# Performance work log

Measured on AMD Instinct MI355X. Metric: run time of the kernel, lower is better.

Reference implementation:

```python
import jax, jax.numpy as jnp
import numpy as np

B, L, C, H, W = 2, 16, 16, 64, 64


def setup_inputs() -> dict:
    key = jax.random.key(0)
    k1, k2 = jax.random.split(key)
    # flows scaled so cumulative normalized-coordinate flows mostly stay in [-1, 1]
    flows = jax.random.normal(k1, (B, L, 2, H, W), dtype=jnp.float32) * 0.05
    images = jax.random.normal(k2, (B, L, C, H, W), dtype=jnp.float32)
    return {"flows": flows, "images": images}


def _bilinear_sample(images, gx, gy):
    # images: [B, Lj, C, H, W]; gx, gy: [B, Li, Lj, H, W] normalized coords in [-1, 1]
    # Replicates torch.nn.functional.grid_sample(mode='bilinear',
    # padding_mode='zeros', align_corners=False).
    Bs, Lj, Cs, Hs, Ws = images.shape
    ix = ((gx + 1.0) * Ws - 1.0) * 0.5  # pixel x coord
    iy = ((gy + 1.0) * Hs - 1.0) * 0.5  # pixel y coord
    x0f = jnp.floor(ix)
    y0f = jnp.floor(iy)
    wx = ix - x0f  # weight toward x0+1 (differentiable w.r.t. flow)
    wy = iy - y0f
    x0 = x0f.astype(jnp.int32)
    y0 = y0f.astype(jnp.int32)
    img_flat = images.reshape(Bs, Lj, Cs, Hs * Ws)

    def gather(xi, yi):
        valid = (xi >= 0) & (xi < Ws) & (yi >= 0) & (yi < Hs)  # [B,Li,Lj,H,W]
        lin = jnp.clip(yi, 0, Hs - 1) * Ws + jnp.clip(xi, 0, Ws - 1)
        lin_t = jnp.transpose(lin, (0, 2, 1, 3, 4))  # [B,Lj,Li,H,W]
        # per (b, j): gather [C, HW] at indices [Li, H, W] -> [C, Li, H, W]
        v = jax.vmap(jax.vmap(lambda im, l: im[:, l]))(img_flat, lin_t)
        v = jnp.transpose(v, (0, 3, 1, 2, 4, 5))  # [B,Li,Lj,C,H,W]
        return v * valid[:, :, :, None, :, :].astype(v.dtype)

    v00 = gather(x0, y0)
    v01 = gather(x0 + 1, y0)
    v10 = gather(x0, y0 + 1)
    v11 = gather(x0 + 1, y0 + 1)
    wX = wx[:, :, :, None, :, :]
    wY = wy[:, :, :, None, :, :]
    return (v00 * (1.0 - wX) * (1.0 - wY) + v01 * wX * (1.0 - wY)
            + v10 * (1.0 - wX) * wY + v11 * wX * wY)


def reference(flows, images):
    Bs, Ls, _, Hs, Ws = flows.shape
    dt = flows.dtype
    cum = jnp.cumsum(flows, axis=1)  # [B,L,2,H,W]
    # rel[b, i, j] = cum[b, i] - cum[b, j]  -> [B,Li,Lj,2,H,W]
    rel = cum[:, :, None] - cum[:, None, :]
    # base sampling grid (pixel centers in normalized coords)
    gx_base = (jnp.arange(Ws, dtype=dt) + 0.5) * (2.0 / Ws) - 1.0  # [W]
    gy_base = (jnp.arange(Hs, dtype=dt) + 0.5) * (2.0 / Hs) - 1.0  # [H]
    gx = gx_base + rel[:, :, :, 0]              # [B,Li,Lj,H,W]
    gy = gy_base[:, None] + rel[:, :, :, 1]     # [B,Li,Lj,H,W]
    gx = jnp.remainder(gx + 1.0, 2.0) - 1.0     # wrap x into [-1, 1)
    warped = _bilinear_sample(images, gx, gy)   # [B,Li,Lj,C,H,W]
    mask = jnp.tril(jnp.ones((Ls, Ls), dtype=dt))
    # causal accumulate over source index j
    return jnp.einsum('bijchw,ij->bichw', warped, mask)
```

## Files before the change

### kernel.cpp

```cpp
#include <hip/hip_runtime.h>

#define BB 2
#define LL 16
#define CC 16
#define HH 64
#define WW 64
#define HWSZ (HH * WW)
#define NSEG 36

__device__ __constant__ int SEG_I[NSEG] = {
    1, 2, 3, 4,
    5, 5, 6, 6, 7, 7, 8, 8,
    9, 9, 9, 10, 10, 10, 11, 11, 11, 12, 12, 12,
    13, 13, 13, 13, 14, 14, 14, 14, 15, 15, 15, 15};
__device__ __constant__ int SEG_J0[NSEG] = {
    0, 0, 0, 0,
    0, 4, 0, 4, 0, 4, 0, 4,
    0, 4, 8, 0, 4, 8, 0, 4, 8, 0, 4, 8,
    0, 4, 8, 12, 0, 4, 8, 12, 0, 4, 8, 12};

#define CUM2_FLOATS (BB * LL * HWSZ * 2)

__global__ __launch_bounds__(256) void gsp_prep(
    const float* __restrict__ flows,
    const float* __restrict__ images,
    float2* __restrict__ cum2,
    float4* __restrict__ nhwc,
    float* __restrict__ out)
{
    if (blockIdx.x < 32) {
        const int gid = blockIdx.x * 256 + threadIdx.x;
        const int b   = gid >> 12;
        const int pix = gid & (HWSZ - 1);
        const float* fb = flows + (size_t)b * LL * 2 * HWSZ + pix;
        float vx[LL], vy[LL];
        #pragma unroll
        for (int l = 0; l < LL; ++l) {
            vx[l] = fb[(size_t)l * 2 * HWSZ];
            vy[l] = fb[(size_t)l * 2 * HWSZ + HWSZ];
        }
        #pragma unroll
        for (int l = 1; l < LL; ++l) { vx[l] += vx[l - 1]; vy[l] += vy[l - 1]; }
        float2* cb = cum2 + (size_t)b * LL * HWSZ + pix;
        #pragma unroll
        for (int l = 0; l < LL; ++l) {
            float2 v; v.x = vx[l]; v.y = vy[l];
            cb[(size_t)l * HWSZ] = v;
        }
    } else {
        const int gid  = (blockIdx.x - 32) * 256 + threadIdx.x;
        const int quad = gid & 3;
        const int pix  = (gid >> 2) & (HWSZ - 1);
        const int bl   = gid >> 14;

        const float* src = images + (size_t)(bl * CC + quad * 4) * HWSZ + pix;
        float4 v;
        v.x = src[0 * HWSZ];
        v.y = src[1 * HWSZ];
        v.z = src[2 * HWSZ];
        v.w = src[3 * HWSZ];
        nhwc[(size_t)(bl * HWSZ + pix) * 4 + quad] = v;

        float* op = out + (size_t)(bl * CC + quad * 4) * HWSZ + pix;
        op[0 * HWSZ] = v.x;
        op[1 * HWSZ] = v.y;
        op[2 * HWSZ] = v.z;
        op[3 * HWSZ] = v.w;
    }
}

__global__ __launch_bounds__(256) void gsp_pairs(
    const float2* __restrict__ cum2,
    const float* __restrict__ nhwc,
    float* __restrict__ out)
{
    const int tile = blockIdx.x & 63;
    const int seg  = (blockIdx.x >> 6) % NSEG;
    const int b    = blockIdx.x / (64 * NSEG);

    const int i    = SEG_I[seg];
    const int j0   = SEG_J0[seg];
    const int jmax = i - 1;

    const int psub = threadIdx.x >> 2;
    const int quad = threadIdx.x & 3;
    const int pix  = tile * 64 + psub;
    const int h = pix >> 6;
    const int w = pix & (WW - 1);

    const float2* cum_b = cum2 + (size_t)b * LL * HWSZ + pix;
    const float* nhwc_b = nhwc + (size_t)b * LL * HWSZ * CC;

    const float gxb = (w + 0.5f) * (2.0f / WW) - 1.0f;
    const float gyb = (h + 0.5f) * (2.0f / HH) - 1.0f;

    const float2 ci = cum_b[(size_t)i * HWSZ];

    float ax = 0.0f, ay = 0.0f, az = 0.0f, aw = 0.0f;

    #pragma unroll
    for (int k = 0; k < 4; ++k) {
        const int jraw = j0 + k;
        const int j = min(jraw, jmax);
        const float wpad = (jraw <= jmax) ? 1.0f : 0.0f;

        const float2 cj = cum_b[(size_t)j * HWSZ];

        float gx = gxb + (ci.x - cj.x);
        float gy = gyb + (ci.y - cj.y);

        float tt = gx + 1.0f;
        tt = tt - floorf(tt * 0.5f) * 2.0f;
        gx = tt - 1.0f;

        const float ix = ((gx + 1.0f) * WW - 1.0f) * 0.5f;
        const float iy = ((gy + 1.0f) * HH - 1.0f) * 0.5f;
        const float x0f = floorf(ix);
        const float y0f = floorf(iy);
        const float fx = ix - x0f;
        const float fy = iy - y0f;
        const int x0 = (int)x0f;
        const int y0 = (int)y0f;
        const int x1 = x0 + 1;
        const int y1 = y0 + 1;

        const bool vx0 = (x0 >= 0) && (x0 < WW);
        const bool vx1 = (x1 >= 0) && (x1 < WW);
        const bool vy0 = (y0 >= 0) && (y0 < HH);
        const bool vy1 = (y1 >= 0) && (y1 < HH);

        const int cx0 = min(max(x0, 0), WW - 1);
        const int cx1 = min(max(x1, 0), WW - 1);
        const int cy0 = min(max(y0, 0), HH - 1);
        const int cy1 = min(max(y1, 0), HH - 1);

        const float w00 = wpad * (1.0f - fx) * (1.0f - fy) * ((vx0 && vy0) ? 1.0f : 0.0f);
        const float w01 = wpad * fx * (1.0f - fy)          * ((vx1 && vy0) ? 1.0f : 0.0f);
        const float w10 = wpad * (1.0f - fx) * fy          * ((vx0 && vy1) ? 1.0f : 0.0f);
        const float w11 = wpad * fx * fy                   * ((vx1 && vy1) ? 1.0f : 0.0f);

        const int o00 = cy0 * WW + cx0;
        const int o01 = cy0 * WW + cx1;
        const int o10 = cy1 * WW + cx0;
        const int o11 = cy1 * WW + cx1;

        const float4* jb = (const float4*)(nhwc_b + (size_t)j * HWSZ * CC);
        const float4 v00 = jb[o00 * 4 + quad];
        const float4 v01 = jb[o01 * 4 + quad];
        const float4 v10 = jb[o10 * 4 + quad];
        const float4 v11 = jb[o11 * 4 + quad];

        ax += w00 * v00.x + w01 * v01.x + w10 * v10.x + w11 * v11.x;
        ay += w00 * v00.y + w01 * v01.y + w10 * v10.y + w11 * v11.y;
        az += w00 * v00.z + w01 * v01.z + w10 * v10.z + w11 * v11.z;
        aw += w00 * v00.w + w01 * v01.w + w10 * v10.w + w11 * v11.w;
    }

    float* op = out + ((size_t)(b * LL + i) * CC + quad * 4) * HWSZ + pix;
    atomicAdd(op + 0 * HWSZ, ax);
    atomicAdd(op + 1 * HWSZ, ay);
    atomicAdd(op + 2 * HWSZ, az);
    atomicAdd(op + 3 * HWSZ, aw);
}

extern "C" void kernel_launch(void* const* d_in, const int* in_sizes, int n_in,
                              void* d_out, int out_size, void* d_ws, size_t ws_size,
                              hipStream_t stream) {
    const float* flows  = (const float*)d_in[0];
    const float* images = (const float*)d_in[1];
    float* out = (float*)d_out;
    float2* cum2 = (float2*)d_ws;
    float*  nhwc = (float*)d_ws + CUM2_FLOATS;

    gsp_prep<<<32 + 2048, 256, 0, stream>>>(flows, images, cum2, (float4*)nhwc, out);

    const int grid = BB * NSEG * 64;
    gsp_pairs<<<grid, 256, 0, stream>>>(cum2, nhwc, out);
}
```

Measured before the change: 91.84 us.

## Stage each source image quarter-plane in LDS and bilinear-gather from shared memory

The pair kernel is replaced by a segment kernel in which each 1024-thread block owns one (batch, target frame, 4-frame source segment, channel quad). For each source frame it copies a 64KB quarter-plane into LDS and does the four bilinear taps from shared memory instead of global/L2. The prep kernel now writes a plane-major quad layout so the block copy is a contiguous stream. In exchange the grid shrinks to 288 large blocks with heavy LDS use and a barrier per source frame. That gives low occupancy, no overlap between the copy and the compute, and a possible tail imbalance across CUs.

```diff
diff --git a/kernel.cpp b/kernel.cpp
--- a/kernel.cpp
+++ b/kernel.cpp
@@ -25,7 +25,7 @@
     const float* __restrict__ flows,
     const float* __restrict__ images,
     float2* __restrict__ cum2,
-    float4* __restrict__ nhwc,
+    float4* __restrict__ qp,
     float* __restrict__ out)
 {
     if (blockIdx.x < 32) {
@@ -59,7 +59,7 @@
         v.y = src[1 * HWSZ];
         v.z = src[2 * HWSZ];
         v.w = src[3 * HWSZ];
-        nhwc[(size_t)(bl * HWSZ + pix) * 4 + quad] = v;
+        qp[((size_t)bl * 4 + quad) * HWSZ + pix] = v;
 
         float* op = out + (size_t)(bl * CC + quad * 4) * HWSZ + pix;
         op[0 * HWSZ] = v.x;
@@ -69,98 +69,102 @@
     }
 }
 
-__global__ __launch_bounds__(256) void gsp_pairs(
+__global__ __launch_bounds__(1024, 8) void gsp_seg(
     const float2* __restrict__ cum2,
-    const float* __restrict__ nhwc,
+    const float4* __restrict__ qp,
     float* __restrict__ out)
 {
-    const int tile = blockIdx.x & 63;
-    const int seg  = (blockIdx.x >> 6) % NSEG;
-    const int b    = blockIdx.x / (64 * NSEG);
+    __shared__ float4 tile[HWSZ];
 
-    const int i    = SEG_I[seg];
-    const int j0   = SEG_J0[seg];
-    const int jmax = i - 1;
+    const int qs  = blockIdx.x & 3;
+    const int seg = (blockIdx.x >> 2) % NSEG;
+    const int b   = blockIdx.x / (4 * NSEG);
 
-    const int psub = threadIdx.x >> 2;
-    const int quad = threadIdx.x & 3;
-    const int pix  = tile * 64 + psub;
-    const int h = pix >> 6;
-    const int w = pix & (WW - 1);
+    const int i  = SEG_I[seg];
+    const int j0 = SEG_J0[seg];
+    const int j1 = min(j0 + 3, i - 1);
 
-    const float2* cum_b = cum2 + (size_t)b * LL * HWSZ + pix;
-    const float* nhwc_b = nhwc + (size_t)b * LL * HWSZ * CC;
+    const float2* cum_b = cum2 + (size_t)b * LL * HWSZ;
 
-    const float gxb = (w + 0.5f) * (2.0f / WW) - 1.0f;
-    const float gyb = (h + 0.5f) * (2.0f / HH) - 1.0f;
-
-    const float2 ci = cum_b[(size_t)i * HWSZ];
-
-    float ax = 0.0f, ay = 0.0f, az = 0.0f, aw = 0.0f;
-
+    float2 ci[4];
+    float4 acc[4];
     #pragma unroll
-    for (int k = 0; k < 4; ++k) {
-        const int jraw = j0 + k;
-        const int j = min(jraw, jmax);
-        const float wpad = (jraw <= jmax) ? 1.0f : 0.0f;
-
-        const float2 cj = cum_b[(size_t)j * HWSZ];
-
-        float gx = gxb + (ci.x - cj.x);
-        float gy = gyb + (ci.y - cj.y);
-
-        float tt = gx + 1.0f;
-        tt = tt - floorf(tt * 0.5f) * 2.0f;
-        gx = tt - 1.0f;
-
-        const float ix = ((gx + 1.0f) * WW - 1.0f) * 0.5f;
-        const float iy = ((gy + 1.0f) * HH - 1.0f) * 0.5f;
-        const float x0f = floorf(ix);
-        const float y0f = floorf(iy);
-        const float fx = ix - x0f;
-        const float fy = iy - y0f;
-        const int x0 = (int)x0f;
-        const int y0 = (int)y0f;
-        const int x1 = x0 + 1;
-        const int y1 = y0 + 1;
-
-        const bool vx0 = (x0 >= 0) && (x0 < WW);
-        const bool vx1 = (x1 >= 0) && (x1 < WW);
-        const bool vy0 = (y0 >= 0) && (y0 < HH);
-        const bool vy1 = (y1 >= 0) && (y1 < HH);
-
-        const int cx0 = min(max(x0, 0), WW - 1);
-        const int cx1 = min(max(x1, 0), WW - 1);
-        const int cy0 = min(max(y0, 0), HH - 1);
-        const int cy1 = min(max(y1, 0), HH - 1);
-
-        const float w00 = wpad * (1.0f - fx) * (1.0f - fy) * ((vx0 && vy0) ? 1.0f : 0.0f);
-        const float w01 = wpad * fx * (1.0f - fy)          * ((vx1 && vy0) ? 1.0f : 0.0f);
-        const float w10 = wpad * (1.0f - fx) * fy          * ((vx0 && vy1) ? 1.0f : 0.0f);
-        const float w11 = wpad * fx * fy                   * ((vx1 && vy1) ? 1.0f : 0.0f);
-
-        const int o00 = cy0 * WW + cx0;
-        const int o01 = cy0 * WW + cx1;
-        const int o10 = cy1 * WW + cx0;
-        const int o11 = cy1 * WW + cx1;
-
-        const float4* jb = (const float4*)(nhwc_b + (size_t)j * HWSZ * CC);
-        const float4 v00 = jb[o00 * 4 + quad];
-        const float4 v01 = jb[o01 * 4 + quad];
-        const float4 v10 = jb[o10 * 4 + quad];
-        const float4 v11 = jb[o11 * 4 + quad];
-
-        ax += w00 * v00.x + w01 * v01.x + w10 * v10.x + w11 * v11.x;
-        ay += w00 * v00.y + w01 * v01.y + w10 * v10.y + w11 * v11.y;
-        az += w00 * v00.z + w01 * v01.z + w10 * v10.z + w11 * v11.z;
-        aw += w00 * v00.w + w01 * v01.w + w10 * v10.w + w11 * v11.w;
+    for (int it = 0; it < 4; ++it) {
+        const int px = threadIdx.x + it * 1024;
+        ci[it] = cum_b[(size_t)i * HWSZ + px];
+        acc[it].x = 0.0f; acc[it].y = 0.0f; acc[it].z = 0.0f; acc[it].w = 0.0f;
     }
 
-    float* op = out + ((size_t)(b * LL + i) * CC + quad * 4) * HWSZ + pix;
-    atomicAdd(op + 0 * HWSZ, ax);
-    atomicAdd(op + 1 * HWSZ, ay);
-    atomicAdd(op + 2 * HWSZ, az);
-    atomicAdd(op + 3 * HWSZ, aw);
+    for (int j = j0; j <= j1; ++j) {
+        const float4* src = qp + ((size_t)(b * LL + j) * 4 + qs) * HWSZ;
+        #pragma unroll
+        for (int it = 0; it < 4; ++it)
+            tile[it * 1024 + threadIdx.x] = src[it * 1024 + threadIdx.x];
+        __syncthreads();
+
+        #pragma unroll
+        for (int it = 0; it < 4; ++it) {
+            const int px = threadIdx.x + it * 1024;
+            const int h = px >> 6;
+            const int w = px & (WW - 1);
+
+            const float2 cj = cum_b[(size_t)j * HWSZ + px];
+
+            float gx = (w + 0.5f) * (2.0f / WW) - 1.0f + (ci[it].x - cj.x);
+            float gy = (h + 0.5f) * (2.0f / HH) - 1.0f + (ci[it].y - cj.y);
+
+            float tt = gx + 1.0f;
+            tt = tt - floorf(tt * 0.5f) * 2.0f;
+            gx = tt - 1.0f;
+
+            const float ix = ((gx + 1.0f) * WW - 1.0f) * 0.5f;
+            const float iy = ((gy + 1.0f) * HH - 1.0f) * 0.5f;
+            const float x0f = floorf(ix);
+            const float y0f = floorf(iy);
+            const float fx = ix - x0f;
+            const float fy = iy - y0f;
+            const int x0 = (int)x0f;
+            const int y0 = (int)y0f;
+            const int x1 = x0 + 1;
+            const int y1 = y0 + 1;
+
+            const bool vx0 = (x0 >= 0) && (x0 < WW);
+            const bool vx1 = (x1 >= 0) && (x1 < WW);
+            const bool vy0 = (y0 >= 0) && (y0 < HH);
+            const bool vy1 = (y1 >= 0) && (y1 < HH);
+
+            const int cx0 = min(max(x0, 0), WW - 1);
+            const int cx1 = min(max(x1, 0), WW - 1);
+            const int cy0 = min(max(y0, 0), HH - 1);
+            const int cy1 = min(max(y1, 0), HH - 1);
+
+            const float w00 = ((vx0 && vy0) ? 1.0f : 0.0f) * (1.0f - fx) * (1.0f - fy);
+            const float w01 = ((vx1 && vy0) ? 1.0f : 0.0f) * fx * (1.0f - fy);
+            const float w10 = ((vx0 && vy1) ? 1.0f : 0.0f) * (1.0f - fx) * fy;
+            const float w11 = ((vx1 && vy1) ? 1.0f : 0.0f) * fx * fy;
+
+            const float4 v00 = tile[cy0 * WW + cx0];
+            const float4 v01 = tile[cy0 * WW + cx1];
+            const float4 v10 = tile[cy1 * WW + cx0];
+            const float4 v11 = tile[cy1 * WW + cx1];
+
+            acc[it].x += w00 * v00.x + w01 * v01.x + w10 * v10.x + w11 * v11.x;
+            acc[it].y += w00 * v00.y + w01 * v01.y + w10 * v10.y + w11 * v11.y;
+            acc[it].z += w00 * v00.z + w01 * v01.z + w10 * v10.z + w11 * v11.z;
+            acc[it].w += w00 * v00.w + w01 * v01.w + w10 * v10.w + w11 * v11.w;
+        }
+        __syncthreads();
+    }
+
+    float* op = out + ((size_t)(b * LL + i) * CC + qs * 4) * HWSZ;
+    #pragma unroll
+    for (int it = 0; it < 4; ++it) {
+        const int px = threadIdx.x + it * 1024;
+        atomicAdd(op + 0 * HWSZ + px, acc[it].x);
+        atomicAdd(op + 1 * HWSZ + px, acc[it].y);
+        atomicAdd(op + 2 * HWSZ + px, acc[it].z);
+        atomicAdd(op + 3 * HWSZ + px, acc[it].w);
+    }
 }
 
 extern "C" void kernel_launch(void* const* d_in, const int* in_sizes, int n_in,
@@ -170,10 +174,10 @@
     const float* images = (const float*)d_in[1];
     float* out = (float*)d_out;
     float2* cum2 = (float2*)d_ws;
-    float*  nhwc = (float*)d_ws + CUM2_FLOATS;
+    float*  qp   = (float*)d_ws + CUM2_FLOATS;
 
-    gsp_prep<<<32 + 2048, 256, 0, stream>>>(flows, images, cum2, (float4*)nhwc, out);
+    gsp_prep<<<32 + 2048, 256, 0, stream>>>(flows, images, cum2, (float4*)qp, out);
 
-    const int grid = BB * NSEG * 64;
-    gsp_pairs<<<grid, 256, 0, stream>>>(cum2, nhwc, out);
+    const int grid = BB * NSEG * 4;
+    gsp_seg<<<grid, 1024, 0, stream>>>(cum2, (const float4*)qp, out);
 }
```

Measured after the change: 100.2 us. 9.1% more time.
